# Kernel optimization log

Measured on AMD Instinct MI355X. Metric: run time of the kernel, lower is better.

The kernel has to match this reference:

```python
import jax, jax.numpy as jnp
import numpy as np

N, M, D0, D1, H, E = 1024, 4096, 1024, 512, 512, 64
TAU = 0.5


def setup_inputs() -> dict:
    key = jax.random.key(0)
    ks = jax.random.split(key, 24)
    g = lambda k, shape, s=0.05: (jax.random.normal(k, shape, jnp.float32) * s)
    # 0/1 meta-path neighbor incidence matrices, avg degree ~16
    nei0 = (jax.random.uniform(ks[0], (N, M)) < 0.004).astype(jnp.float32)
    nei1 = (jax.random.uniform(ks[1], (N, M)) < 0.004).astype(jnp.float32)
    def norm_adj(k):
        a = (jax.random.uniform(k, (N, N)) < 0.005).astype(jnp.float32) + jnp.eye(N, dtype=jnp.float32)
        return a / a.sum(1, keepdims=True)
    return dict(
        feat0=g(ks[2], (N, D0), 1.0), feat1=g(ks[3], (M, D1), 1.0), feat2=g(ks[4], (M, D1), 1.0),
        mask_feat=g(ks[5], (N, D0), 1.0),
        nei0=nei0, nei1=nei1,
        adj0=norm_adj(ks[6]), adj1=norm_adj(ks[7]),
        madj0=norm_adj(ks[8]), madj1=norm_adj(ks[9]),
        fc0_w=g(ks[10], (D0, H)), fc0_b=jnp.zeros((H,), jnp.float32),
        fc1_w=g(ks[11], (D1, H)), fc1_b=jnp.zeros((H,), jnp.float32),
        fc2_w=g(ks[12], (D1, H)), fc2_b=jnp.zeros((H,), jnp.float32),
        agg0_w=g(ks[13], (H, H)), agg1_w=g(ks[14], (H, H)),
        gcn_w1=g(ks[15], (H, E)), gcn_b1=jnp.zeros((E,), jnp.float32),
        gcn_w2=g(ks[16], (E, E)), gcn_b2=jnp.zeros((E,), jnp.float32),
        att_w=g(ks[17], (E, E)), att_b=jnp.zeros((E,), jnp.float32),
        att_vec=g(ks[18], (E,)),
        proj_w=g(ks[19], (E, E)), proj_b=jnp.zeros((E,), jnp.float32),
        mlp1_w=g(ks[20], (E, 16)), mlp1_b=jnp.zeros((16,), jnp.float32),
        mlp2_w=g(ks[21], (16, 1)), mlp2_b=jnp.zeros((1,), jnp.float32),
    )


def _l2norm(x):
    # F.normalize(dim=1)
    return x / jnp.maximum(jnp.linalg.norm(x, axis=1, keepdims=True), 1e-12)


def reference(feat0, feat1, feat2, mask_feat, nei0, nei1, adj0, adj1, madj0, madj1,
              fc0_w, fc0_b, fc1_w, fc1_b, fc2_w, fc2_b, agg0_w, agg1_w,
              gcn_w1, gcn_b1, gcn_w2, gcn_b2, att_w, att_b, att_vec,
              proj_w, proj_b, mlp1_w, mlp1_b, mlp2_w, mlp2_b):
    elu = jax.nn.elu
    # aggregate_nei_acm (dropout in eval mode => identity)
    h_tar = elu(feat0 @ fc0_w + fc0_b)                       # [N, H]
    h_mask = elu(mask_feat @ fc0_w + fc0_b)                  # [N, H]
    h_nei = [elu(feat1 @ fc1_w + fc1_b), elu(feat2 @ fc2_w + fc2_b)]  # [M, H]
    neis = [nei0, nei1]
    agg_ws = [agg0_w, agg1_w]
    views, masks = [], []
    for i in range(2):
        cnt = jnp.maximum(neis[i].sum(1, keepdims=True), 1.0)  # nei_index_count, clamped >0
        h_agg = (neis[i] @ h_nei[i]) / cnt                     # sparse neighbor mean, [N, H]
        t = h_agg @ agg_ws[i]
        views.append(elu(h_tar + t))
        masks.append(elu(h_mask + t))

    def gcn(x, adj):
        # 2-layer GCN: relu(A X W1 + b1) -> A H W2 + b2
        h = jax.nn.relu(adj @ (x @ gcn_w1) + gcn_b1)
        return adj @ (h @ gcn_w2) + gcn_b2

    mean_adj = (adj0 + adj1) * 0.5                           # torch.stack(adjs).mean(0)
    z_coarse = gcn(h_tar, mean_adj)                          # [N, E]
    # order: Encoder(view_i, adj_i), Encoder(mask_i, mask_adj_i) per i
    h_fine = [gcn(views[0], adj0), gcn(masks[0], madj0),
              gcn(views[1], adj1), gcn(masks[1], madj1)]
    hs = jnp.stack([_l2norm(h) for h in h_fine])             # [V=4, N, E]
    # semantic attention over views
    e = jnp.einsum('vne,e->v', jnp.tanh(hs @ att_w + att_b), att_vec) / hs.shape[1]
    beta = jax.nn.softmax(e)
    z_fine = jnp.einsum('v,vne->ne', beta, hs)               # [N, E]
    zc = _l2norm(jnp.tanh(z_coarse @ proj_w + proj_b))
    zf = _l2norm(jnp.tanh(z_fine @ proj_w + proj_b))
    # weight_InfoNce
    logits = (zf @ zc.T) / TAU                               # [N, N]
    dots = jnp.exp(logits)
    pair = zf[:, None, :] + zc[None, :, :]                   # [N, N, E] = z_anchor[i] + z[j]
    w = jax.nn.sigmoid(jnp.tanh(pair @ mlp1_w + mlp1_b) @ mlp2_w + mlp2_b)[..., 0]
    denom = jnp.sum(dots * w, axis=1)
    # -log(diag(dots)/denom) = log(denom) - diag(logits)
    loss = jnp.mean(jnp.log(denom) - jnp.diagonal(logits))
    return loss
```

## Files before the change

kernel.cpp:

```cpp
#include <hip/hip_runtime.h>

#define ACT_NONE 0
#define ACT_ELU  1
#define ACT_RELU 2
#define ACT_TANH 3

typedef __attribute__((ext_vector_type(8))) short short8;
typedef __attribute__((ext_vector_type(4))) float f32x4;

__device__ __forceinline__ float frcp(float x) { return __builtin_amdgcn_rcpf(x); }
__device__ __forceinline__ float fexp(float x) { return __expf(x); }
__device__ __forceinline__ float ftanh(float x) {
    return 1.f - 2.f * frcp(fexp(2.f * x) + 1.f);
}
__device__ __forceinline__ float fsigmoid(float x) {
    return frcp(1.f + fexp(-x));
}

__device__ __forceinline__ float apply_act(float v, int act) {
    if (act == ACT_ELU)  return v > 0.f ? v : fexp(v) - 1.f;
    if (act == ACT_RELU) return fmaxf(v, 0.f);
    if (act == ACT_TANH) return ftanh(v);
    return v;
}

__device__ __forceinline__ unsigned short f2bf(float f) {
    unsigned int u = __float_as_uint(f);
    unsigned int r = (u + 0x7fffu + ((u >> 16) & 1u)) >> 16;
    return (unsigned short)r;
}
__device__ __forceinline__ float bf2f(unsigned short u) {
    return __uint_as_float(((unsigned int)u) << 16);
}

#define GLOAD16(gp, lp) __builtin_amdgcn_global_load_lds( \
    (const __attribute__((address_space(1))) void*)(gp),  \
    (__attribute__((address_space(3))) void*)(lp), 16, 0, 0)

struct CTDesc { const float* in; unsigned short* out; int R, C, tcols, tile0; };
struct CMDesc { const float* in; unsigned short* out; int start4; };
struct CastArr {
    CTDesc t[10]; int nt; int T;
    CMDesc f[6]; int nf; int total4;
};

__global__ __launch_bounds__(256) void cast_all_kernel(CastArr a) {
    int b = blockIdx.x;
    if (b < a.T) {
        int s = 0;
        while (s + 1 < a.nt && b >= a.t[s + 1].tile0) ++s;
        const CTDesc d = a.t[s];
        int lt = b - d.tile0;
        int tr = lt / d.tcols, tc = lt % d.tcols;
        int r0 = tr * 32, c0 = tc * 32;
        __shared__ float tt[32][33];
        int tx = threadIdx.x & 31, ty = threadIdx.x >> 5;
        for (int i = ty; i < 32; i += 8) {
            int r = r0 + i, c = c0 + tx;
            tt[i][tx] = (r < d.R && c < d.C) ? d.in[(size_t)r * d.C + c] : 0.f;
        }
        __syncthreads();
        for (int i = ty; i < 32; i += 8) {
            int c = c0 + i, r = r0 + tx;
            if (c < d.C && r < d.R) d.out[(size_t)c * d.R + r] = f2bf(tt[tx][i]);
        }
    } else {
        int g4 = (b - a.T) * 256 + threadIdx.x;
        if (g4 >= a.total4) return;
        int s = 0;
        while (s + 1 < a.nf && g4 >= a.f[s + 1].start4) ++s;
        int l4 = g4 - a.f[s].start4;
        float4 v = *reinterpret_cast<const float4*>(a.f[s].in + (size_t)l4 * 4);
        ushort4 o;
        o.x = f2bf(v.x); o.y = f2bf(v.y); o.z = f2bf(v.z); o.w = f2bf(v.w);
        *reinterpret_cast<ushort4*>(a.f[s].out + (size_t)l4 * 4) = o;
    }
}

__global__ __launch_bounds__(256) void gemm128_kernel(
    const unsigned short* __restrict__ A, const unsigned short* __restrict__ Bt,
    const unsigned short* __restrict__ Bt2, int m_split,
    const float* __restrict__ bias, const float* __restrict__ bias2,
    float* __restrict__ C, unsigned short* __restrict__ Cbf, int cbf_mlimit,
    int M, int K, int N, int act) {
    __shared__ unsigned short As[8 * 512];
    __shared__ unsigned short Bs[8 * 512];
    const int tid = threadIdx.x;
    const int w = tid >> 6, lane = tid & 63;
    const int wr = w >> 1, wc = w & 1;
    const int lr = lane & 15, lk = lane >> 4;
    const int bm = blockIdx.y * 128, bn = blockIdx.x * 128;
    const unsigned short* Bu = Bt;
    const float* bu = bias;
    if (bm >= m_split) { Bu = Bt2; bu = bias2; }

    const unsigned short* ga0 = A  + (size_t)(bm + (2 * w)     * 16 + lr) * K + lk * 8;
    const unsigned short* ga1 = A  + (size_t)(bm + (2 * w + 1) * 16 + lr) * K + lk * 8;
    const unsigned short* gb0 = Bu + (size_t)(bn + (2 * w)     * 16 + lr) * K + lk * 8;
    const unsigned short* gb1 = Bu + (size_t)(bn + (2 * w + 1) * 16 + lr) * K + lk * 8;
    unsigned short* la0 = &As[(2 * w) * 512];
    unsigned short* la1 = &As[(2 * w + 1) * 512];
    unsigned short* lb0 = &Bs[(2 * w) * 512];
    unsigned short* lb1 = &Bs[(2 * w + 1) * 512];

    f32x4 acc[4][4] = {};
    for (int k0 = 0; k0 < K; k0 += 32) {
        GLOAD16(ga0 + k0, la0);
        GLOAD16(ga1 + k0, la1);
        GLOAD16(gb0 + k0, lb0);
        GLOAD16(gb1 + k0, lb1);
        __syncthreads();
        short8 a[4], b[4];
        #pragma unroll
        for (int i = 0; i < 4; ++i)
            a[i] = *reinterpret_cast<const short8*>(&As[(4 * wr + i) * 512 + lane * 8]);
        #pragma unroll
        for (int j = 0; j < 4; ++j)
            b[j] = *reinterpret_cast<const short8*>(&Bs[(4 * wc + j) * 512 + lane * 8]);
        #pragma unroll
        for (int i = 0; i < 4; ++i)
            #pragma unroll
            for (int j = 0; j < 4; ++j)
                acc[i][j] = __builtin_amdgcn_mfma_f32_16x16x32_bf16(a[i], b[j], acc[i][j], 0, 0, 0);
        __syncthreads();
    }
    #pragma unroll
    for (int i = 0; i < 4; ++i) {
        #pragma unroll
        for (int j = 0; j < 4; ++j) {
            int gcol = bn + wc * 64 + j * 16 + lr;
            float bv = bu ? bu[gcol] : 0.f;
            #pragma unroll
            for (int r = 0; r < 4; ++r) {
                int grow = bm + wr * 64 + i * 16 + lk * 4 + r;
                float v = apply_act(acc[i][j][r] + bv, act);
                if (C)   C[(size_t)grow * N + gcol] = v;
                if (Cbf && grow < cbf_mlimit) Cbf[(size_t)grow * N + gcol] = f2bf(v);
            }
        }
    }
}

__global__ __launch_bounds__(256) void gemm_bf16_kernel(
    const unsigned short* __restrict__ A, const unsigned short* __restrict__ Bt,
    const float* __restrict__ bias,
    float* __restrict__ C, unsigned short* __restrict__ Cbf, int cbf_mlimit,
    int M, int K, int N, int act) {
    const int tid = threadIdx.x;
    const int w = tid >> 6, lane = tid & 63;
    const int wr = w >> 1, wc = w & 1;
    const int lr = lane & 15, lk = lane >> 4;
    const int bm = blockIdx.y * 64, bn = blockIdx.x * 64;

    const int arow0 = bm + wr * 32 + lr;
    const int brow0 = bn + wc * 32 + lr;

    f32x4 acc[2][2] = {};
    const short8 zero8 = {};
    #pragma unroll 4
    for (int k0 = 0; k0 < K; k0 += 32) {
        short8 a[2], b[2];
        #pragma unroll
        for (int i = 0; i < 2; ++i)
            a[i] = *reinterpret_cast<const short8*>(&A[(size_t)(arow0 + i * 16) * K + k0 + lk * 8]);
        #pragma unroll
        for (int j = 0; j < 2; ++j) {
            int br = brow0 + j * 16;
            b[j] = (br < N) ? *reinterpret_cast<const short8*>(&Bt[(size_t)br * K + k0 + lk * 8])
                            : zero8;
        }
        #pragma unroll
        for (int i = 0; i < 2; ++i)
            #pragma unroll
            for (int j = 0; j < 2; ++j)
                acc[i][j] = __builtin_amdgcn_mfma_f32_16x16x32_bf16(a[i], b[j], acc[i][j], 0, 0, 0);
    }
    #pragma unroll
    for (int i = 0; i < 2; ++i) {
        #pragma unroll
        for (int j = 0; j < 2; ++j) {
            int gcol = bn + wc * 32 + j * 16 + lr;
            if (gcol >= N) continue;
            float bv = bias ? bias[gcol] : 0.f;
            #pragma unroll
            for (int r = 0; r < 4; ++r) {
                int grow = bm + wr * 32 + i * 16 + lk * 4 + r;
                float v = apply_act(acc[i][j][r] + bv, act);
                if (C)   C[(size_t)grow * N + gcol] = v;
                if (Cbf && grow < cbf_mlimit) Cbf[(size_t)grow * N + gcol] = f2bf(v);
            }
        }
    }
}

__global__ __launch_bounds__(256) void neiagg_kernel(
    const float* __restrict__ nei0, const float* __restrict__ nei1,
    const unsigned short* __restrict__ hn0, const unsigned short* __restrict__ hn1,
    unsigned short* __restrict__ hagg) {
    const int row = blockIdx.x, br = blockIdx.y, t = threadIdx.x;
    const float* nei = br ? nei1 : nei0;
    const unsigned short* hn = br ? hn1 : hn0;
    __shared__ int idxs[256];
    __shared__ int cnt;
    if (t == 0) cnt = 0;
    __syncthreads();
    const float4* nr = reinterpret_cast<const float4*>(nei + (size_t)row * 4096);
    for (int j = t; j < 1024; j += 256) {
        float4 v = nr[j];
        if (v.x != 0.f) { int s = atomicAdd(&cnt, 1); if (s < 256) idxs[s] = j * 4 + 0; }
        if (v.y != 0.f) { int s = atomicAdd(&cnt, 1); if (s < 256) idxs[s] = j * 4 + 1; }
        if (v.z != 0.f) { int s = atomicAdd(&cnt, 1); if (s < 256) idxs[s] = j * 4 + 2; }
        if (v.w != 0.f) { int s = atomicAdd(&cnt, 1); if (s < 256) idxs[s] = j * 4 + 3; }
    }
    __syncthreads();
    int n = cnt < 256 ? cnt : 256;
    float inv = frcp(fmaxf((float)cnt, 1.f));
    int c = t * 2;
    float a0 = 0.f, a1 = 0.f, b0 = 0.f, b1 = 0.f;
    int k = 0;
    for (; k + 2 <= n; k += 2) {
        ushort2 u = *reinterpret_cast<const ushort2*>(&hn[(size_t)idxs[k] * 512 + c]);
        ushort2 v = *reinterpret_cast<const ushort2*>(&hn[(size_t)idxs[k + 1] * 512 + c]);
        a0 += bf2f(u.x); a1 += bf2f(u.y);
        b0 += bf2f(v.x); b1 += bf2f(v.y);
    }
    if (k < n) {
        ushort2 u = *reinterpret_cast<const ushort2*>(&hn[(size_t)idxs[k] * 512 + c]);
        a0 += bf2f(u.x); a1 += bf2f(u.y);
    }
    ushort2 o; o.x = f2bf((a0 + b0) * inv); o.y = f2bf((a1 + b1) * inv);
    *reinterpret_cast<ushort2*>(&hagg[((size_t)br * 1024 + row) * 512 + c]) = o;
}

__global__ void addelu_kernel(const float* __restrict__ ht, const float* __restrict__ hm,
                              const float* __restrict__ tt, unsigned short* __restrict__ xcat,
                              int nh) {
    int idx = blockIdx.x * 256 + threadIdx.x;
    if (idx < nh) {
        float h1 = ht[idx], h2 = hm[idx];
        float t0 = tt[idx], t1 = tt[idx + nh];
        float a = h1 + t0, b = h2 + t0, c = h1 + t1, d = h2 + t1;
        xcat[(size_t)1 * nh + idx] = f2bf(a > 0.f ? a : fexp(a) - 1.f);
        xcat[(size_t)2 * nh + idx] = f2bf(b > 0.f ? b : fexp(b) - 1.f);
        xcat[(size_t)3 * nh + idx] = f2bf(c > 0.f ? c : fexp(c) - 1.f);
        xcat[(size_t)4 * nh + idx] = f2bf(d > 0.f ? d : fexp(d) - 1.f);
    }
}

__global__ __launch_bounds__(64) void adjprep_kernel(
    const float* __restrict__ adj0, const float* __restrict__ adj1,
    const float* __restrict__ madj0, const float* __restrict__ madj1,
    int* __restrict__ cnts, int* __restrict__ idxs, float* __restrict__ wts) {
    const int row = blockIdx.x, br = blockIdx.y, t = threadIdx.x;
    const float* Aa; const float* Ab = nullptr; float sc = 1.f;
    if (br == 0)      { Aa = adj0; Ab = adj1; sc = 0.5f; }
    else if (br == 1) { Aa = adj0; }
    else if (br == 2) { Aa = madj0; }
    else if (br == 3) { Aa = adj1; }
    else              { Aa = madj1; }
    __shared__ int li[128];
    __shared__ float lw[128];
    __shared__ int cnt;
    if (t == 0) cnt = 0;
    __syncthreads();
    const float4* ar = reinterpret_cast<const float4*>(Aa + (size_t)row * 1024);
    const float4* brp = Ab ? reinterpret_cast<const float4*>(Ab + (size_t)row * 1024) : nullptr;
    for (int j = t; j < 256; j += 64) {
        float4 v = ar[j];
        if (brp) { float4 u = brp[j]; v.x += u.x; v.y += u.y; v.z += u.z; v.w += u.w; }
        if (v.x != 0.f) { int s = atomicAdd(&cnt, 1); if (s < 128) { li[s] = j * 4 + 0; lw[s] = v.x * sc; } }
        if (v.y != 0.f) { int s = atomicAdd(&cnt, 1); if (s < 128) { li[s] = j * 4 + 1; lw[s] = v.y * sc; } }
        if (v.z != 0.f) { int s = atomicAdd(&cnt, 1); if (s < 128) { li[s] = j * 4 + 2; lw[s] = v.z * sc; } }
        if (v.w != 0.f) { int s = atomicAdd(&cnt, 1); if (s < 128) { li[s] = j * 4 + 3; lw[s] = v.w * sc; } }
    }
    __syncthreads();
    int n = cnt < 128 ? cnt : 128;
    size_t base = ((size_t)br * 1024 + row) * 128;
    for (int k = t; k < n; k += 64) { idxs[base + k] = li[k]; wts[base + k] = lw[k]; }
    if (t == 0) cnts[br * 1024 + row] = n;
}

__device__ __forceinline__ float sparse_gather(const int* __restrict__ idxs,
                                               const float* __restrict__ wts,
                                               size_t base, int n,
                                               const float* __restrict__ Xb, int t,
                                               float acc) {
    float a1 = 0.f, a2 = 0.f, a3 = 0.f;
    int k = 0;
    for (; k + 4 <= n; k += 4) {
        int   i0 = idxs[base + k],     i1 = idxs[base + k + 1];
        int   i2 = idxs[base + k + 2], i3 = idxs[base + k + 3];
        float w0 = wts[base + k],      w1 = wts[base + k + 1];
        float w2 = wts[base + k + 2],  w3 = wts[base + k + 3];
        acc += w0 * Xb[(size_t)i0 * 64 + t];
        a1  += w1 * Xb[(size_t)i1 * 64 + t];
        a2  += w2 * Xb[(size_t)i2 * 64 + t];
        a3  += w3 * Xb[(size_t)i3 * 64 + t];
    }
    for (; k < n; ++k) acc += wts[base + k] * Xb[(size_t)idxs[base + k] * 64 + t];
    return acc + a1 + a2 + a3;
}

__global__ __launch_bounds__(256) void spmm1_kernel(
    const int* __restrict__ cnts, const int* __restrict__ idxs, const float* __restrict__ wts,
    const float* __restrict__ X, const float* __restrict__ bias,
    unsigned short* __restrict__ out) {
    const int row = blockIdx.x * 4 + (threadIdx.x >> 6);
    const int br = blockIdx.y, t = threadIdx.x & 63;
    size_t base = ((size_t)br * 1024 + row) * 128;
    int n = cnts[br * 1024 + row];
    float acc = sparse_gather(idxs, wts, base, n, X + (size_t)br * 1024 * 64, t, bias[t]);
    out[((size_t)br * 1024 + row) * 64 + t] = f2bf(fmaxf(acc, 0.f));
}

__global__ __launch_bounds__(256) void spmm2_kernel(
    const int* __restrict__ cnts, const int* __restrict__ idxs, const float* __restrict__ wts,
    const float* __restrict__ X, const float* __restrict__ bias,
    unsigned short* __restrict__ zcf_bf, float* __restrict__ hs,
    const float* __restrict__ att_w, const float* __restrict__ att_b,
    const float* __restrict__ att_vec, float* __restrict__ att_row) {
    const int wv = threadIdx.x >> 6;
    const int row = blockIdx.x * 4 + wv;
    const int br = blockIdx.y, t = threadIdx.x & 63;
    size_t base = ((size_t)br * 1024 + row) * 128;
    int n = cnts[br * 1024 + row];
    float acc = sparse_gather(idxs, wts, base, n, X + (size_t)br * 1024 * 64, t, bias[t]);
    if (br == 0) {
        zcf_bf[(size_t)row * 64 + t] = f2bf(acc);
        return;
    }
    float s = acc * acc;
    #pragma unroll
    for (int o = 32; o; o >>= 1) s += __shfl_down(s, o);
    s = __shfl(s, 0);
    float v = acc * frcp(fmaxf(sqrtf(s), 1e-12f));
    hs[((size_t)(br - 1) * 1024 + row) * 64 + t] = v;
    __shared__ float rs[4][64];
    rs[wv][t] = v;
    float sa = att_b[t];
    #pragma unroll
    for (int k = 0; k < 64; ++k) sa += rs[wv][k] * att_w[k * 64 + t];
    float val = ftanh(sa) * att_vec[t];
    #pragma unroll
    for (int o = 32; o; o >>= 1) val += __shfl_down(val, o);
    if (t == 0) att_row[(size_t)(br - 1) * 1024 + row] = val;
}

__global__ __launch_bounds__(256) void attreduce_kernel(const float* __restrict__ att_row,
                                                        float* __restrict__ small) {
    const int v = blockIdx.x, t = threadIdx.x;
    const float* p = att_row + (size_t)v * 1024;
    float s = p[t] + p[t + 256] + p[t + 512] + p[t + 768];
    #pragma unroll
    for (int o = 32; o; o >>= 1) s += __shfl_down(s, o);
    __shared__ float ps[4];
    if ((t & 63) == 0) ps[t >> 6] = s;
    __syncthreads();
    if (t == 0) small[v] = ps[0] + ps[1] + ps[2] + ps[3];
}

__global__ void zfine_kernel(const float* __restrict__ hs, const float* __restrict__ small,
                             unsigned short* __restrict__ out) {
    int idx = blockIdx.x * 256 + threadIdx.x;
    if (idx < 65536) {
        float e0 = small[0] * (1.f / 1024.f), e1 = small[1] * (1.f / 1024.f);
        float e2 = small[2] * (1.f / 1024.f), e3 = small[3] * (1.f / 1024.f);
        float mx = fmaxf(fmaxf(e0, e1), fmaxf(e2, e3));
        float x0 = expf(e0 - mx), x1 = expf(e1 - mx), x2 = expf(e2 - mx), x3 = expf(e3 - mx);
        float inv = 1.f / (x0 + x1 + x2 + x3);
        float v = (x0 * hs[idx] + x1 * hs[idx + 65536] +
                   x2 * hs[idx + 131072] + x3 * hs[idx + 196608]) * inv;
        out[idx] = f2bf(v);
    }
}

__global__ __launch_bounds__(256) void l2normA1_kernel(float* __restrict__ X,
                                                       const unsigned short* __restrict__ mlp1_wT,
                                                       float* __restrict__ AC1) {
    const int wv = threadIdx.x >> 6;
    const int row = blockIdx.x * 4 + wv;
    const int t = threadIdx.x & 63;
    float v = X[(size_t)row * 64 + t];
    float s = v * v;
    #pragma unroll
    for (int o = 32; o; o >>= 1) s += __shfl_down(s, o);
    s = __shfl(s, 0);
    float r = v * frcp(fmaxf(sqrtf(s), 1e-12f));
    X[(size_t)row * 64 + t] = r;
    __shared__ float zs[4][64];
    zs[wv][t] = r;
    if (t < 16) {
        float acc = 0.f;
        #pragma unroll
        for (int e = 0; e < 64; ++e) acc += zs[wv][e] * bf2f(mlp1_wT[t * 64 + e]);
        AC1[(size_t)row * 16 + t] = acc;
    }
}

__global__ __launch_bounds__(256) void infonce_kernel(
    const float* __restrict__ zf, const float* __restrict__ zc,
    const float* __restrict__ A1, const float* __restrict__ C1,
    const float* __restrict__ b1, const float* __restrict__ m2,
    const float* __restrict__ b2v, float* __restrict__ loss_acc) {
    const int i0 = blockIdx.x * 4, t = threadIdx.x;
    __shared__ __align__(16) float zfs[4][64];
    __shared__ float a1b[4][16], m2s[16];
    __shared__ float diag[4];
    __shared__ float wsum[4][4];
    if (t < 64) {
        #pragma unroll
        for (int ii = 0; ii < 4; ++ii) zfs[ii][t] = zf[(size_t)(i0 + ii) * 64 + t];
    }
    if (t < 16) {
        float bb = b1[t];
        #pragma unroll
        for (int ii = 0; ii < 4; ++ii) a1b[ii][t] = A1[(size_t)(i0 + ii) * 16 + t] + bb;
        m2s[t] = m2[t];
    }
    __syncthreads();
    const float b2 = b2v[0];
    float acc[4] = {};
    for (int j = t; j < 1024; j += 256) {
        const float4* zcj = reinterpret_cast<const float4*>(zc + (size_t)j * 64);
        float dot[4] = {};
        #pragma unroll
        for (int e = 0; e < 16; ++e) {
            float4 b = zcj[e];
            #pragma unroll
            for (int ii = 0; ii < 4; ++ii) {
                float4 a = reinterpret_cast<const float4*>(zfs[ii])[e];
                dot[ii] += a.x * b.x + a.y * b.y + a.z * b.z + a.w * b.w;
            }
        }
        float c1j[16];
        #pragma unroll
        for (int q = 0; q < 4; ++q) {
            float4 c4 = reinterpret_cast<const float4*>(C1 + (size_t)j * 16)[q];
            c1j[q * 4 + 0] = c4.x; c1j[q * 4 + 1] = c4.y;
            c1j[q * 4 + 2] = c4.z; c1j[q * 4 + 3] = c4.w;
        }
        #pragma unroll
        for (int ii = 0; ii < 4; ++ii) {
            float logit = dot[ii] * 2.0f;
            float h = b2;
            #pragma unroll
            for (int k = 0; k < 16; ++k) h += ftanh(a1b[ii][k] + c1j[k]) * m2s[k];
            acc[ii] += fexp(logit) * fsigmoid(h);
            if (j == i0 + ii) diag[ii] = logit;
        }
    }
    #pragma unroll
    for (int ii = 0; ii < 4; ++ii) {
        float a = acc[ii];
        #pragma unroll
        for (int o = 32; o; o >>= 1) a += __shfl_down(a, o);
        if ((t & 63) == 0) wsum[t >> 6][ii] = a;
    }
    __syncthreads();
    if (t == 0) {
        float part = 0.f;
        #pragma unroll
        for (int ii = 0; ii < 4; ++ii) {
            float denom = wsum[0][ii] + wsum[1][ii] + wsum[2][ii] + wsum[3][ii];
            part += logf(denom) - diag[ii];
        }
        atomicAdd(loss_acc, part);
    }
}

__global__ void finalize_kernel(const float* __restrict__ small, float* __restrict__ out) {
    if (threadIdx.x == 0) out[0] = small[4] * (1.f / 1024.f);
}

extern "C" void kernel_launch(void* const* d_in, const int* in_sizes, int n_in,
                              void* d_out, int out_size, void* d_ws, size_t ws_size,
                              hipStream_t stream) {
    const float* feat0     = (const float*)d_in[0];
    const float* feat1     = (const float*)d_in[1];
    const float* feat2     = (const float*)d_in[2];
    const float* mask_feat = (const float*)d_in[3];
    const float* nei0      = (const float*)d_in[4];
    const float* nei1      = (const float*)d_in[5];
    const float* adj0      = (const float*)d_in[6];
    const float* adj1      = (const float*)d_in[7];
    const float* madj0     = (const float*)d_in[8];
    const float* madj1     = (const float*)d_in[9];
    const float* fc0_w = (const float*)d_in[10];
    const float* fc0_b = (const float*)d_in[11];
    const float* fc1_w = (const float*)d_in[12];
    const float* fc1_b = (const float*)d_in[13];
    const float* fc2_w = (const float*)d_in[14];
    const float* fc2_b = (const float*)d_in[15];
    const float* agg0_w = (const float*)d_in[16];
    const float* agg1_w = (const float*)d_in[17];
    const float* gcn_w1 = (const float*)d_in[18];
    const float* gcn_b1 = (const float*)d_in[19];
    const float* gcn_w2 = (const float*)d_in[20];
    const float* gcn_b2 = (const float*)d_in[21];
    const float* att_w  = (const float*)d_in[22];
    const float* att_b  = (const float*)d_in[23];
    const float* att_vec = (const float*)d_in[24];
    const float* proj_w = (const float*)d_in[25];
    const float* proj_b = (const float*)d_in[26];
    const float* mlp1_w = (const float*)d_in[27];
    const float* mlp1_b = (const float*)d_in[28];
    const float* mlp2_w = (const float*)d_in[29];
    const float* mlp2_b = (const float*)d_in[30];

    const int N = 1024, M = 4096, D0 = 1024, D1 = 512, H = 512, E = 64;
    typedef unsigned short bf;

    float* W = (float*)d_ws;
    size_t off = 0;
    auto allocf = [&](size_t n) { float* p = W + off; off += n; return p; };
    float* h_tar   = allocf((size_t)N * H);
    float* h_mask  = allocf((size_t)N * H);
    float* tbuf    = allocf((size_t)2 * N * H);
    float* xw1cat  = allocf((size_t)5 * N * E);
    float* hw2cat  = allocf((size_t)5 * N * E);
    float* hs      = allocf((size_t)4 * N * E);
    float* zcat    = allocf((size_t)2 * N * E);
    float* AC1     = allocf((size_t)2 * N * 16);
    float* att_row = allocf((size_t)4 * N);
    float* small   = allocf(16);
    float* adj_wts = allocf((size_t)5 * 1024 * 128);
    int*   adj_idx = (int*)allocf((size_t)5 * 1024 * 128);
    int*   adj_cnt = (int*)allocf((size_t)5 * 1024);
    bf* BP = (bf*)(W + off);
    size_t boff = 0;
    auto allocb = [&](size_t n) { bf* p = BP + boff; boff += n; return p; };
    bf* feat0_bf = allocb((size_t)N * D0);
    bf* mask_bf  = allocb((size_t)N * D0);
    bf* feat1_bf = allocb((size_t)M * D1);
    bf* feat2_bf = allocb((size_t)M * D1);
    bf* xcat_bf  = allocb((size_t)5 * N * H);
    bf* hnei0_bf = allocb((size_t)M * H);
    bf* hnei1_bf = allocb((size_t)M * H);
    bf* hagg_bf  = allocb((size_t)2 * N * H);
    bf* h1cat_bf = allocb((size_t)5 * N * E);
    bf* zcf_bf   = allocb((size_t)2 * N * E);
    bf* fc0_wT  = allocb((size_t)H * D0);
    bf* fc1_wT  = allocb((size_t)H * D1);
    bf* fc2_wT  = allocb((size_t)H * D1);
    bf* agg0_wT = allocb((size_t)H * H);
    bf* agg1_wT = allocb((size_t)H * H);
    bf* gw1_T   = allocb((size_t)E * H);
    bf* gw2_T   = allocb((size_t)E * E);
    bf* proj_wT = allocb((size_t)E * E);
    bf* mlp1_wT = allocb((size_t)16 * E);

    auto gemm128 = [&](const bf* A, const bf* Bt, const bf* Bt2, int msplit,
                       const float* bias, const float* bias2, float* C, bf* Cbf, int cbf_lim,
                       int Mm, int Kk, int Nn, int act) {
        dim3 g(Nn / 128, Mm / 128);
        gemm128_kernel<<<g, 256, 0, stream>>>(A, Bt, Bt2, msplit, bias, bias2,
                                              C, Cbf, cbf_lim, Mm, Kk, Nn, act);
    };
    auto gemm64 = [&](const bf* A, const bf* Bt, const float* bias, float* C, bf* Cbf,
                      int cbf_lim, int Mm, int Kk, int Nn, int act) {
        dim3 g((Nn + 63) / 64, Mm / 64);
        gemm_bf16_kernel<<<g, 256, 0, stream>>>(A, Bt, bias, C, Cbf, cbf_lim, Mm, Kk, Nn, act);
    };

    hipMemsetAsync((void*)small, 0, 16 * sizeof(float), stream);

    {
        CastArr a; int tile = 0, i = 0;
        auto addT = [&](const float* in, bf* out, int R, int C) {
            int tc = (C + 31) / 32, trn = (R + 31) / 32;
            a.t[i++] = CTDesc{in, out, R, C, tc, tile};
            tile += tc * trn;
        };
        addT(fc0_w, fc0_wT, D0, H);
        addT(fc1_w, fc1_wT, D1, H);
        addT(fc2_w, fc2_wT, D1, H);
        addT(agg0_w, agg0_wT, H, H);
        addT(agg1_w, agg1_wT, H, H);
        addT(gcn_w1, gw1_T, H, E);
        addT(gcn_w2, gw2_T, E, E);
        addT(proj_w, proj_wT, E, E);
        addT(mlp1_w, mlp1_wT, E, 16);
        a.nt = i; a.T = tile;
        int s4 = 0, fi = 0;
        auto addF = [&](const float* in, bf* out, int n) {
            a.f[fi++] = CMDesc{in, out, s4}; s4 += n / 4;
        };
        addF(feat0, feat0_bf, N * D0);
        addF(mask_feat, mask_bf, N * D0);
        addF(feat1, feat1_bf, M * D1);
        addF(feat2, feat2_bf, M * D1);
        a.nf = fi; a.total4 = s4;
        int nb = tile + (s4 + 255) / 256;
        cast_all_kernel<<<nb, 256, 0, stream>>>(a);
    }
    adjprep_kernel<<<dim3(N, 5), 64, 0, stream>>>(adj0, adj1, madj0, madj1,
                                                  adj_cnt, adj_idx, adj_wts);

    gemm128(feat0_bf, fc0_wT, nullptr, 1 << 30, fc0_b, nullptr,
            h_tar, xcat_bf, N, 2 * N, D0, H, ACT_ELU);
    gemm128(feat1_bf, fc1_wT, fc2_wT, M, fc1_b, fc2_b,
            nullptr, hnei0_bf, 2 * M, 2 * M, D1, H, ACT_ELU);

    neiagg_kernel<<<dim3(N, 2), 256, 0, stream>>>(nei0, nei1, hnei0_bf, hnei1_bf, hagg_bf);
    gemm128(hagg_bf, agg0_wT, agg1_wT, N, nullptr, nullptr,
            tbuf, nullptr, 0, 2 * N, H, H, ACT_NONE);
    addelu_kernel<<<(N * H + 255) / 256, 256, 0, stream>>>(h_tar, h_mask, tbuf, xcat_bf, N * H);

    gemm64(xcat_bf, gw1_T, nullptr, xw1cat, nullptr, 0, 5 * N, H, E, ACT_NONE);
    spmm1_kernel<<<dim3(N / 4, 5), 256, 0, stream>>>(adj_cnt, adj_idx, adj_wts, xw1cat, gcn_b1, h1cat_bf);
    gemm64(h1cat_bf, gw2_T, nullptr, hw2cat, nullptr, 0, 5 * N, E, E, ACT_NONE);
    spmm2_kernel<<<dim3(N / 4, 5), 256, 0, stream>>>(adj_cnt, adj_idx, adj_wts, hw2cat, gcn_b2,
                                                     zcf_bf, hs, att_w, att_b, att_vec, att_row);
    attreduce_kernel<<<4, 256, 0, stream>>>(att_row, small);

    zfine_kernel<<<(N * E + 255) / 256, 256, 0, stream>>>(hs, small, zcf_bf + (size_t)N * E);

    gemm64(zcf_bf, proj_wT, proj_b, zcat, nullptr, 0, 2 * N, E, E, ACT_TANH);
    l2normA1_kernel<<<2 * N / 4, 256, 0, stream>>>(zcat, mlp1_wT, AC1);

    const float* zc = zcat;
    const float* zf = zcat + (size_t)N * E;
    const float* C1 = AC1;
    const float* A1 = AC1 + (size_t)N * 16;
    infonce_kernel<<<N / 4, 256, 0, stream>>>(zf, zc, A1, C1, mlp1_b, mlp2_w, mlp2_b, small + 4);

    finalize_kernel<<<1, 64, 0, stream>>>(small, (float*)d_out);
}
```

Measured before the change: 325.4 us.

## Merge input GEMMs, split-K small GEMMs, fuse small matmuls into sparse/projection kernels

Replaces the LDS-staged 128x128 GEMM with a segmented 64x64 direct-load GEMM so the two input projections run in one launch. The aggregation and GCN-W1 GEMMs become split-K with two partial buffers, which are summed in addelu and spmm1. The 64x64 GCN-W2 matmul is folded into spmm2, and z_fine, projection, tanh, normalisation and the MLP1 precompute are merged into one projhead kernel. The goal is fewer launches and more parallelism for small-N GEMMs. In exchange, the large GEMMs lose LDS tiling reuse and per-row scalar FP32 matmuls replace MFMA for the small layers.

```diff
diff --git a/kernel.cpp b/kernel.cpp
--- a/kernel.cpp
+++ b/kernel.cpp
@@ -33,14 +33,10 @@
     return __uint_as_float(((unsigned int)u) << 16);
 }
 
-#define GLOAD16(gp, lp) __builtin_amdgcn_global_load_lds( \
-    (const __attribute__((address_space(1))) void*)(gp),  \
-    (__attribute__((address_space(3))) void*)(lp), 16, 0, 0)
-
 struct CTDesc { const float* in; unsigned short* out; int R, C, tcols, tile0; };
 struct CMDesc { const float* in; unsigned short* out; int start4; };
 struct CastArr {
-    CTDesc t[10]; int nt; int T;
+    CTDesc t[8]; int nt; int T;
     CMDesc f[6]; int nf; int total4;
 };
 
@@ -77,98 +73,100 @@
     }
 }
 
-__global__ __launch_bounds__(256) void gemm128_kernel(
-    const unsigned short* __restrict__ A, const unsigned short* __restrict__ Bt,
-    const unsigned short* __restrict__ Bt2, int m_split,
-    const float* __restrict__ bias, const float* __restrict__ bias2,
-    float* __restrict__ C, unsigned short* __restrict__ Cbf, int cbf_mlimit,
-    int M, int K, int N, int act) {
-    __shared__ unsigned short As[8 * 512];
-    __shared__ unsigned short Bs[8 * 512];
+struct GSeg {
+    const unsigned short* A;
+    const unsigned short* Bt;
+    const unsigned short* Bt2;
+    const float* bias;
+    const float* bias2;
+    float* C;
+    unsigned short* Cbf;
+    int cbf_mlimit;
+    int m_split;
+    int K;
+    int act;
+    int mt0;
+};
+struct GArr { GSeg s[2]; int ns; int N; };
+
+__global__ __launch_bounds__(256) void gemm_seg_kernel(GArr g) {
+    const int mt = blockIdx.y;
+    const int si = (g.ns > 1 && mt >= g.s[1].mt0) ? 1 : 0;
+    const GSeg s = g.s[si];
+    const int K = s.K, N = g.N;
     const int tid = threadIdx.x;
     const int w = tid >> 6, lane = tid & 63;
     const int wr = w >> 1, wc = w & 1;
     const int lr = lane & 15, lk = lane >> 4;
-    const int bm = blockIdx.y * 128, bn = blockIdx.x * 128;
-    const unsigned short* Bu = Bt;
-    const float* bu = bias;
-    if (bm >= m_split) { Bu = Bt2; bu = bias2; }
-
-    const unsigned short* ga0 = A  + (size_t)(bm + (2 * w)     * 16 + lr) * K + lk * 8;
-    const unsigned short* ga1 = A  + (size_t)(bm + (2 * w + 1) * 16 + lr) * K + lk * 8;
-    const unsigned short* gb0 = Bu + (size_t)(bn + (2 * w)     * 16 + lr) * K + lk * 8;
-    const unsigned short* gb1 = Bu + (size_t)(bn + (2 * w + 1) * 16 + lr) * K + lk * 8;
-    unsigned short* la0 = &As[(2 * w) * 512];
-    unsigned short* la1 = &As[(2 * w + 1) * 512];
-    unsigned short* lb0 = &Bs[(2 * w) * 512];
-    unsigned short* lb1 = &Bs[(2 * w + 1) * 512];
-
-    f32x4 acc[4][4] = {};
+    const int bm = (mt - s.mt0) * 64, bn = blockIdx.x * 64;
+    const unsigned short* Bu = s.Bt;
+    const float* bu = s.bias;
+    if (bm >= s.m_split) { Bu = s.Bt2; bu = s.bias2; }
+
+    const int arow0 = bm + wr * 32 + lr;
+    const int brow0 = bn + wc * 32 + lr;
+
+    f32x4 acc[2][2] = {};
+    #pragma unroll 4
     for (int k0 = 0; k0 < K; k0 += 32) {
-        GLOAD16(ga0 + k0, la0);
-        GLOAD16(ga1 + k0, la1);
-        GLOAD16(gb0 + k0, lb0);
-        GLOAD16(gb1 + k0, lb1);
-        __syncthreads();
-        short8 a[4], b[4];
-        #pragma unroll
-        for (int i = 0; i < 4; ++i)
-            a[i] = *reinterpret_cast<const short8*>(&As[(4 * wr + i) * 512 + lane * 8]);
-        #pragma unroll
-        for (int j = 0; j < 4; ++j)
-            b[j] = *reinterpret_cast<const short8*>(&Bs[(4 * wc + j) * 512 + lane * 8]);
-        #pragma unroll
-        for (int i = 0; i < 4; ++i)
+        short8 a[2], b[2];
+        #pragma unroll
+        for (int i = 0; i < 2; ++i)
+            a[i] = *reinterpret_cast<const short8*>(&s.A[(size_t)(arow0 + i * 16) * K + k0 + lk * 8]);
+        #pragma unroll
+        for (int j = 0; j < 2; ++j)
+            b[j] = *reinterpret_cast<const short8*>(&Bu[(size_t)(brow0 + j * 16) * K + k0 + lk * 8]);
+        #pragma unroll
+        for (int i = 0; i < 2; ++i)
             #pragma unroll
-            for (int j = 0; j < 4; ++j)
+            for (int j = 0; j < 2; ++j)
                 acc[i][j] = __builtin_amdgcn_mfma_f32_16x16x32_bf16(a[i], b[j], acc[i][j], 0, 0, 0);
-        __syncthreads();
-    }
-    #pragma unroll
-    for (int i = 0; i < 4; ++i) {
-        #pragma unroll
-        for (int j = 0; j < 4; ++j) {
-            int gcol = bn + wc * 64 + j * 16 + lr;
+    }
+    #pragma unroll
+    for (int i = 0; i < 2; ++i) {
+        #pragma unroll
+        for (int j = 0; j < 2; ++j) {
+            int gcol = bn + wc * 32 + j * 16 + lr;
             float bv = bu ? bu[gcol] : 0.f;
             #pragma unroll
             for (int r = 0; r < 4; ++r) {
-                int grow = bm + wr * 64 + i * 16 + lk * 4 + r;
-                float v = apply_act(acc[i][j][r] + bv, act);
-                if (C)   C[(size_t)grow * N + gcol] = v;
-                if (Cbf && grow < cbf_mlimit) Cbf[(size_t)grow * N + gcol] = f2bf(v);
+                int grow = bm + wr * 32 + i * 16 + lk * 4 + r;
+                float v = apply_act(acc[i][j][r] + bv, s.act);
+                if (s.C)   s.C[(size_t)grow * N + gcol] = v;
+                if (s.Cbf && grow < s.cbf_mlimit) s.Cbf[(size_t)grow * N + gcol] = f2bf(v);
             }
         }
     }
 }
 
-__global__ __launch_bounds__(256) void gemm_bf16_kernel(
+__global__ __launch_bounds__(256) void gemm_splitk_kernel(
     const unsigned short* __restrict__ A, const unsigned short* __restrict__ Bt,
-    const float* __restrict__ bias,
-    float* __restrict__ C, unsigned short* __restrict__ Cbf, int cbf_mlimit,
-    int M, int K, int N, int act) {
+    const unsigned short* __restrict__ Bt2, int m_split,
+    float* __restrict__ C, int M, int K, int N, int ksplit) {
     const int tid = threadIdx.x;
     const int w = tid >> 6, lane = tid & 63;
     const int wr = w >> 1, wc = w & 1;
     const int lr = lane & 15, lk = lane >> 4;
     const int bm = blockIdx.y * 64, bn = blockIdx.x * 64;
+    const int z = blockIdx.z;
+    const int kbeg = z * ksplit;
+    const int kend = kbeg + ksplit < K ? kbeg + ksplit : K;
+    C += (size_t)z * M * N;
+    const unsigned short* Bu = (bm >= m_split) ? Bt2 : Bt;
 
     const int arow0 = bm + wr * 32 + lr;
     const int brow0 = bn + wc * 32 + lr;
 
     f32x4 acc[2][2] = {};
-    const short8 zero8 = {};
     #pragma unroll 4
-    for (int k0 = 0; k0 < K; k0 += 32) {
+    for (int k0 = kbeg; k0 < kend; k0 += 32) {
         short8 a[2], b[2];
         #pragma unroll
         for (int i = 0; i < 2; ++i)
             a[i] = *reinterpret_cast<const short8*>(&A[(size_t)(arow0 + i * 16) * K + k0 + lk * 8]);
         #pragma unroll
-        for (int j = 0; j < 2; ++j) {
-            int br = brow0 + j * 16;
-            b[j] = (br < N) ? *reinterpret_cast<const short8*>(&Bt[(size_t)br * K + k0 + lk * 8])
-                            : zero8;
-        }
+        for (int j = 0; j < 2; ++j)
+            b[j] = *reinterpret_cast<const short8*>(&Bu[(size_t)(brow0 + j * 16) * K + k0 + lk * 8]);
         #pragma unroll
         for (int i = 0; i < 2; ++i)
             #pragma unroll
@@ -176,21 +174,16 @@
                 acc[i][j] = __builtin_amdgcn_mfma_f32_16x16x32_bf16(a[i], b[j], acc[i][j], 0, 0, 0);
     }
     #pragma unroll
-    for (int i = 0; i < 2; ++i) {
+    for (int i = 0; i < 2; ++i)
         #pragma unroll
         for (int j = 0; j < 2; ++j) {
             int gcol = bn + wc * 32 + j * 16 + lr;
-            if (gcol >= N) continue;
-            float bv = bias ? bias[gcol] : 0.f;
             #pragma unroll
             for (int r = 0; r < 4; ++r) {
                 int grow = bm + wr * 32 + i * 16 + lk * 4 + r;
-                float v = apply_act(acc[i][j][r] + bv, act);
-                if (C)   C[(size_t)grow * N + gcol] = v;
-                if (Cbf && grow < cbf_mlimit) Cbf[(size_t)grow * N + gcol] = f2bf(v);
+                C[(size_t)grow * N + gcol] = acc[i][j][r];
             }
         }
-    }
 }
 
 __global__ __launch_bounds__(256) void neiagg_kernel(
@@ -234,11 +227,12 @@
 
 __global__ void addelu_kernel(const float* __restrict__ ht, const float* __restrict__ hm,
                               const float* __restrict__ tt, unsigned short* __restrict__ xcat,
-                              int nh) {
+                              int nh, int PL) {
     int idx = blockIdx.x * 256 + threadIdx.x;
     if (idx < nh) {
         float h1 = ht[idx], h2 = hm[idx];
-        float t0 = tt[idx], t1 = tt[idx + nh];
+        float t0 = tt[idx] + tt[idx + PL];
+        float t1 = tt[idx + nh] + tt[idx + nh + PL];
         float a = h1 + t0, b = h2 + t0, c = h1 + t1, d = h2 + t1;
         xcat[(size_t)1 * nh + idx] = f2bf(a > 0.f ? a : fexp(a) - 1.f);
         xcat[(size_t)2 * nh + idx] = f2bf(b > 0.f ? b : fexp(b) - 1.f);
@@ -280,69 +274,77 @@
     if (t == 0) cnts[br * 1024 + row] = n;
 }
 
-__device__ __forceinline__ float sparse_gather(const int* __restrict__ idxs,
-                                               const float* __restrict__ wts,
-                                               size_t base, int n,
-                                               const float* __restrict__ Xb, int t,
-                                               float acc) {
-    float a1 = 0.f, a2 = 0.f, a3 = 0.f;
-    int k = 0;
-    for (; k + 4 <= n; k += 4) {
-        int   i0 = idxs[base + k],     i1 = idxs[base + k + 1];
-        int   i2 = idxs[base + k + 2], i3 = idxs[base + k + 3];
-        float w0 = wts[base + k],      w1 = wts[base + k + 1];
-        float w2 = wts[base + k + 2],  w3 = wts[base + k + 3];
-        acc += w0 * Xb[(size_t)i0 * 64 + t];
-        a1  += w1 * Xb[(size_t)i1 * 64 + t];
-        a2  += w2 * Xb[(size_t)i2 * 64 + t];
-        a3  += w3 * Xb[(size_t)i3 * 64 + t];
-    }
-    for (; k < n; ++k) acc += wts[base + k] * Xb[(size_t)idxs[base + k] * 64 + t];
-    return acc + a1 + a2 + a3;
-}
-
 __global__ __launch_bounds__(256) void spmm1_kernel(
     const int* __restrict__ cnts, const int* __restrict__ idxs, const float* __restrict__ wts,
-    const float* __restrict__ X, const float* __restrict__ bias,
+    const float* __restrict__ X, int PL, const float* __restrict__ bias,
     unsigned short* __restrict__ out) {
     const int row = blockIdx.x * 4 + (threadIdx.x >> 6);
     const int br = blockIdx.y, t = threadIdx.x & 63;
     size_t base = ((size_t)br * 1024 + row) * 128;
     int n = cnts[br * 1024 + row];
-    float acc = sparse_gather(idxs, wts, base, n, X + (size_t)br * 1024 * 64, t, bias[t]);
+    const float* Xb = X + (size_t)br * 1024 * 64;
+    const float* Xb2 = Xb + PL;
+    float acc = bias[t], a1 = 0.f;
+    int k = 0;
+    for (; k + 2 <= n; k += 2) {
+        int   i0 = idxs[base + k], i1 = idxs[base + k + 1];
+        float w0 = wts[base + k],  w1 = wts[base + k + 1];
+        acc += w0 * (Xb[(size_t)i0 * 64 + t] + Xb2[(size_t)i0 * 64 + t]);
+        a1  += w1 * (Xb[(size_t)i1 * 64 + t] + Xb2[(size_t)i1 * 64 + t]);
+    }
+    if (k < n) {
+        int i0 = idxs[base + k];
+        acc += wts[base + k] * (Xb[(size_t)i0 * 64 + t] + Xb2[(size_t)i0 * 64 + t]);
+    }
+    acc += a1;
     out[((size_t)br * 1024 + row) * 64 + t] = f2bf(fmaxf(acc, 0.f));
 }
 
 __global__ __launch_bounds__(256) void spmm2_kernel(
     const int* __restrict__ cnts, const int* __restrict__ idxs, const float* __restrict__ wts,
-    const float* __restrict__ X, const float* __restrict__ bias,
-    unsigned short* __restrict__ zcf_bf, float* __restrict__ hs,
-    const float* __restrict__ att_w, const float* __restrict__ att_b,
-    const float* __restrict__ att_vec, float* __restrict__ att_row) {
+    const unsigned short* __restrict__ H1, const float* __restrict__ w2,
+    const float* __restrict__ b2, unsigned short* __restrict__ zcf_bf,
+    float* __restrict__ hs, const float* __restrict__ att_w,
+    const float* __restrict__ att_b, const float* __restrict__ att_vec,
+    float* __restrict__ att_row) {
     const int wv = threadIdx.x >> 6;
     const int row = blockIdx.x * 4 + wv;
     const int br = blockIdx.y, t = threadIdx.x & 63;
     size_t base = ((size_t)br * 1024 + row) * 128;
     int n = cnts[br * 1024 + row];
-    float acc = sparse_gather(idxs, wts, base, n, X + (size_t)br * 1024 * 64, t, bias[t]);
+    const unsigned short* Hb = H1 + (size_t)br * 1024 * 64;
+    float g0 = 0.f, g1 = 0.f, g2 = 0.f, g3 = 0.f;
+    int k = 0;
+    for (; k + 4 <= n; k += 4) {
+        g0 += wts[base + k]     * bf2f(Hb[(size_t)idxs[base + k]     * 64 + t]);
+        g1 += wts[base + k + 1] * bf2f(Hb[(size_t)idxs[base + k + 1] * 64 + t]);
+        g2 += wts[base + k + 2] * bf2f(Hb[(size_t)idxs[base + k + 2] * 64 + t]);
+        g3 += wts[base + k + 3] * bf2f(Hb[(size_t)idxs[base + k + 3] * 64 + t]);
+    }
+    for (; k < n; ++k) g0 += wts[base + k] * bf2f(Hb[(size_t)idxs[base + k] * 64 + t]);
+    float g = (g0 + g1) + (g2 + g3);
+    __shared__ float rs[4][64];
+    rs[wv][t] = g;
+    float o = b2[t];
+    #pragma unroll
+    for (int c = 0; c < 64; ++c) o += rs[wv][c] * w2[c * 64 + t];
     if (br == 0) {
-        zcf_bf[(size_t)row * 64 + t] = f2bf(acc);
+        zcf_bf[(size_t)row * 64 + t] = f2bf(o);
         return;
     }
-    float s = acc * acc;
-    #pragma unroll
-    for (int o = 32; o; o >>= 1) s += __shfl_down(s, o);
+    float s = o * o;
+    #pragma unroll
+    for (int q = 32; q; q >>= 1) s += __shfl_down(s, q);
     s = __shfl(s, 0);
-    float v = acc * frcp(fmaxf(sqrtf(s), 1e-12f));
+    float v = o * frcp(fmaxf(sqrtf(s), 1e-12f));
     hs[((size_t)(br - 1) * 1024 + row) * 64 + t] = v;
-    __shared__ float rs[4][64];
     rs[wv][t] = v;
     float sa = att_b[t];
     #pragma unroll
-    for (int k = 0; k < 64; ++k) sa += rs[wv][k] * att_w[k * 64 + t];
+    for (int c = 0; c < 64; ++c) sa += rs[wv][c] * att_w[c * 64 + t];
     float val = ftanh(sa) * att_vec[t];
     #pragma unroll
-    for (int o = 32; o; o >>= 1) val += __shfl_down(val, o);
+    for (int q = 32; q; q >>= 1) val += __shfl_down(val, q);
     if (t == 0) att_row[(size_t)(br - 1) * 1024 + row] = val;
 }
 
@@ -359,41 +361,46 @@
     if (t == 0) small[v] = ps[0] + ps[1] + ps[2] + ps[3];
 }
 
-__global__ void zfine_kernel(const float* __restrict__ hs, const float* __restrict__ small,
-                             unsigned short* __restrict__ out) {
-    int idx = blockIdx.x * 256 + threadIdx.x;
-    if (idx < 65536) {
+__global__ __launch_bounds__(256) void projhead_kernel(
+    const unsigned short* __restrict__ zcf_bf, const float* __restrict__ hs,
+    const float* __restrict__ small, const float* __restrict__ proj_w,
+    const float* __restrict__ proj_b, const float* __restrict__ mlp1_w,
+    float* __restrict__ zcat, float* __restrict__ AC1) {
+    const int wv = threadIdx.x >> 6;
+    const int row = blockIdx.x * 4 + wv;
+    const int t = threadIdx.x & 63;
+    float zv;
+    if (row < 1024) {
+        zv = bf2f(zcf_bf[(size_t)row * 64 + t]);
+    } else {
+        int r = row - 1024;
         float e0 = small[0] * (1.f / 1024.f), e1 = small[1] * (1.f / 1024.f);
         float e2 = small[2] * (1.f / 1024.f), e3 = small[3] * (1.f / 1024.f);
         float mx = fmaxf(fmaxf(e0, e1), fmaxf(e2, e3));
         float x0 = expf(e0 - mx), x1 = expf(e1 - mx), x2 = expf(e2 - mx), x3 = expf(e3 - mx);
         float inv = 1.f / (x0 + x1 + x2 + x3);
-        float v = (x0 * hs[idx] + x1 * hs[idx + 65536] +
-                   x2 * hs[idx + 131072] + x3 * hs[idx + 196608]) * inv;
-        out[idx] = f2bf(v);
-    }
-}
-
-__global__ __launch_bounds__(256) void l2normA1_kernel(float* __restrict__ X,
-                                                       const unsigned short* __restrict__ mlp1_wT,
-                                                       float* __restrict__ AC1) {
-    const int wv = threadIdx.x >> 6;
-    const int row = blockIdx.x * 4 + wv;
-    const int t = threadIdx.x & 63;
-    float v = X[(size_t)row * 64 + t];
-    float s = v * v;
-    #pragma unroll
-    for (int o = 32; o; o >>= 1) s += __shfl_down(s, o);
+        size_t ix = (size_t)r * 64 + t;
+        zv = (x0 * hs[ix] + x1 * hs[ix + 65536] +
+              x2 * hs[ix + 131072] + x3 * hs[ix + 196608]) * inv;
+    }
+    __shared__ float rs[4][64];
+    rs[wv][t] = zv;
+    float p = proj_b[t];
+    #pragma unroll
+    for (int c = 0; c < 64; ++c) p += rs[wv][c] * proj_w[c * 64 + t];
+    p = ftanh(p);
+    float s = p * p;
+    #pragma unroll
+    for (int q = 32; q; q >>= 1) s += __shfl_down(s, q);
     s = __shfl(s, 0);
-    float r = v * frcp(fmaxf(sqrtf(s), 1e-12f));
-    X[(size_t)row * 64 + t] = r;
-    __shared__ float zs[4][64];
-    zs[wv][t] = r;
+    float r = p * frcp(fmaxf(sqrtf(s), 1e-12f));
+    zcat[(size_t)row * 64 + t] = r;
+    rs[wv][t] = r;
     if (t < 16) {
-        float acc = 0.f;
-        #pragma unroll
-        for (int e = 0; e < 64; ++e) acc += zs[wv][e] * bf2f(mlp1_wT[t * 64 + e]);
-        AC1[(size_t)row * 16 + t] = acc;
+        float a = 0.f;
+        #pragma unroll
+        for (int c = 0; c < 64; ++c) a += rs[wv][c] * mlp1_w[c * 16 + t];
+        AC1[(size_t)row * 16 + t] = a;
     }
 }
 
@@ -515,9 +522,8 @@
     auto allocf = [&](size_t n) { float* p = W + off; off += n; return p; };
     float* h_tar   = allocf((size_t)N * H);
     float* h_mask  = allocf((size_t)N * H);
-    float* tbuf    = allocf((size_t)2 * N * H);
-    float* xw1cat  = allocf((size_t)5 * N * E);
-    float* hw2cat  = allocf((size_t)5 * N * E);
+    float* tbuf    = allocf((size_t)2 * 2 * N * H);
+    float* xw1cat  = allocf((size_t)2 * 5 * N * E);
     float* hs      = allocf((size_t)4 * N * E);
     float* zcat    = allocf((size_t)2 * N * E);
     float* AC1     = allocf((size_t)2 * N * 16);
@@ -538,29 +544,13 @@
     bf* hnei1_bf = allocb((size_t)M * H);
     bf* hagg_bf  = allocb((size_t)2 * N * H);
     bf* h1cat_bf = allocb((size_t)5 * N * E);
-    bf* zcf_bf   = allocb((size_t)2 * N * E);
+    bf* zcf_bf   = allocb((size_t)N * E);
     bf* fc0_wT  = allocb((size_t)H * D0);
     bf* fc1_wT  = allocb((size_t)H * D1);
     bf* fc2_wT  = allocb((size_t)H * D1);
     bf* agg0_wT = allocb((size_t)H * H);
     bf* agg1_wT = allocb((size_t)H * H);
     bf* gw1_T   = allocb((size_t)E * H);
-    bf* gw2_T   = allocb((size_t)E * E);
-    bf* proj_wT = allocb((size_t)E * E);
-    bf* mlp1_wT = allocb((size_t)16 * E);
-
-    auto gemm128 = [&](const bf* A, const bf* Bt, const bf* Bt2, int msplit,
-                       const float* bias, const float* bias2, float* C, bf* Cbf, int cbf_lim,
-                       int Mm, int Kk, int Nn, int act) {
-        dim3 g(Nn / 128, Mm / 128);
-        gemm128_kernel<<<g, 256, 0, stream>>>(A, Bt, Bt2, msplit, bias, bias2,
-                                              C, Cbf, cbf_lim, Mm, Kk, Nn, act);
-    };
-    auto gemm64 = [&](const bf* A, const bf* Bt, const float* bias, float* C, bf* Cbf,
-                      int cbf_lim, int Mm, int Kk, int Nn, int act) {
-        dim3 g((Nn + 63) / 64, Mm / 64);
-        gemm_bf16_kernel<<<g, 256, 0, stream>>>(A, Bt, bias, C, Cbf, cbf_lim, Mm, Kk, Nn, act);
-    };
 
     hipMemsetAsync((void*)small, 0, 16 * sizeof(float), stream);
 
@@ -577,9 +567,6 @@
         addT(agg0_w, agg0_wT, H, H);
         addT(agg1_w, agg1_wT, H, H);
         addT(gcn_w1, gw1_T, H, E);
-        addT(gcn_w2, gw2_T, E, E);
-        addT(proj_w, proj_wT, E, E);
-        addT(mlp1_w, mlp1_wT, E, 16);
         a.nt = i; a.T = tile;
         int s4 = 0, fi = 0;
         auto addF = [&](const float* in, bf* out, int n) {
@@ -596,27 +583,33 @@
     adjprep_kernel<<<dim3(N, 5), 64, 0, stream>>>(adj0, adj1, madj0, madj1,
                                                   adj_cnt, adj_idx, adj_wts);
 
-    gemm128(feat0_bf, fc0_wT, nullptr, 1 << 30, fc0_b, nullptr,
-            h_tar, xcat_bf, N, 2 * N, D0, H, ACT_ELU);
-    gemm128(feat1_bf, fc1_wT, fc2_wT, M, fc1_b, fc2_b,
-            nullptr, hnei0_bf, 2 * M, 2 * M, D1, H, ACT_ELU);
+    {
+        GArr g;
+        g.s[0] = GSeg{feat0_bf, fc0_wT, nullptr, fc0_b, nullptr,
+                      h_tar, xcat_bf, N, 1 << 30, D0, ACT_ELU, 0};
+        g.s[1] = GSeg{feat1_bf, fc1_wT, fc2_wT, fc1_b, fc2_b,
+                      nullptr, hnei0_bf, 2 * M, M, D1, ACT_ELU, 32};
+        g.ns = 2; g.N = H;
+        gemm_seg_kernel<<<dim3(H / 64, 32 + 128), 256, 0, stream>>>(g);
+    }
 
     neiagg_kernel<<<dim3(N, 2), 256, 0, stream>>>(nei0, nei1, hnei0_bf, hnei1_bf, hagg_bf);
-    gemm128(hagg_bf, agg0_wT, agg1_wT, N, nullptr, nullptr,
-            tbuf, nullptr, 0, 2 * N, H, H, ACT_NONE);
-    addelu_kernel<<<(N * H + 255) / 256, 256, 0, stream>>>(h_tar, h_mask, tbuf, xcat_bf, N * H);
-
-    gemm64(xcat_bf, gw1_T, nullptr, xw1cat, nullptr, 0, 5 * N, H, E, ACT_NONE);
-    spmm1_kernel<<<dim3(N / 4, 5), 256, 0, stream>>>(adj_cnt, adj_idx, adj_wts, xw1cat, gcn_b1, h1cat_bf);
-    gemm64(h1cat_bf, gw2_T, nullptr, hw2cat, nullptr, 0, 5 * N, E, E, ACT_NONE);
-    spmm2_kernel<<<dim3(N / 4, 5), 256, 0, stream>>>(adj_cnt, adj_idx, adj_wts, hw2cat, gcn_b2,
-                                                     zcf_bf, hs, att_w, att_b, att_vec, att_row);
+    gemm_splitk_kernel<<<dim3(H / 64, 2 * N / 64, 2), 256, 0, stream>>>(
+        hagg_bf, agg0_wT, agg1_wT, N, tbuf, 2 * N, H, H, 256);
+    addelu_kernel<<<(N * H + 255) / 256, 256, 0, stream>>>(h_tar, h_mask, tbuf, xcat_bf,
+                                                           N * H, 2 * N * H);
+
+    gemm_splitk_kernel<<<dim3(1, 5 * N / 64, 2), 256, 0, stream>>>(
+        xcat_bf, gw1_T, nullptr, 1 << 30, xw1cat, 5 * N, H, E, 256);
+    spmm1_kernel<<<dim3(N / 4, 5), 256, 0, stream>>>(adj_cnt, adj_idx, adj_wts,
+                                                     xw1cat, 5 * N * E, gcn_b1, h1cat_bf);
+    spmm2_kernel<<<dim3(N / 4, 5), 256, 0, stream>>>(adj_cnt, adj_idx, adj_wts, h1cat_bf,
+                                                     gcn_w2, gcn_b2, zcf_bf, hs,
+                                                     att_w, att_b, att_vec, att_row);
     attreduce_kernel<<<4, 256, 0, stream>>>(att_row, small);
 
-    zfine_kernel<<<(N * E + 255) / 256, 256, 0, stream>>>(hs, small, zcf_bf + (size_t)N * E);
-
-    gemm64(zcf_bf, proj_wT, proj_b, zcat, nullptr, 0, 2 * N, E, E, ACT_TANH);
-    l2normA1_kernel<<<2 * N / 4, 256, 0, stream>>>(zcat, mlp1_wT, AC1);
+    projhead_kernel<<<2 * N / 4, 256, 0, stream>>>(zcf_bf, hs, small, proj_w, proj_b,
+                                                   mlp1_w, zcat, AC1);
 
     const float* zc = zcat;
     const float* zf = zcat + (size_t)N * E;
```

Measured after the change: 289.3 us. 11.1% less time.
